# Kernel optimization log

Measured on AMD Instinct MI355X. Metric: run time of the kernel, lower is better.

The kernel has to match this reference:

```python
import jax, jax.numpy as jnp
import numpy as np

N_NODES = 100000


def _add_self_loops(edge_index, n):
    loops = jnp.arange(n, dtype=edge_index.dtype)
    src = jnp.concatenate([edge_index[0], loops])
    dst = jnp.concatenate([edge_index[1], loops])
    return src, dst


def _gcn_norm(src, dst, n):
    # symmetric normalization with unit edge weights (edge_weight=None)
    w = jnp.ones(src.shape[0], dtype=jnp.float32)
    deg = jax.ops.segment_sum(w, dst, num_segments=n)  # in-degree at dst (col)
    dinv = jnp.where(deg > 0, jax.lax.rsqrt(jnp.maximum(deg, 1.0)), 0.0)
    return dinv[src] * w * dinv[dst]


def _gcn_conv(x, W, b, src, dst, norm, n):
    h = x @ W                              # [N, F_out] linear first (as in PyG GCNConv)
    msg = h[src] * norm[:, None]           # gather + per-edge scale
    agg = jax.ops.segment_sum(msg, dst, num_segments=n)  # scatter-add at dst
    return agg + b


def setup_inputs() -> dict:
    key = jax.random.key(0)
    k1, k2, k3, k4 = jax.random.split(key, 4)
    x = jax.random.normal(k1, (N_NODES, 128), dtype=jnp.float32)
    edge_index = jax.random.randint(k2, (2, 1600000), 0, N_NODES, dtype=jnp.int64)
    W1 = jax.random.normal(k3, (128, 64), dtype=jnp.float32) * 0.08
    b1 = jnp.zeros((64,), dtype=jnp.float32)
    W2 = jax.random.normal(k4, (64, 40), dtype=jnp.float32) * 0.1
    b2 = jnp.zeros((40,), dtype=jnp.float32)
    return {"x": x, "edge_index": edge_index, "W1": W1, "b1": b1, "W2": W2, "b2": b2}


def reference(x, edge_index, W1, b1, W2, b2):
    n = x.shape[0]
    src, dst = _add_self_loops(edge_index, n)
    norm = _gcn_norm(src, dst, n)
    h = _gcn_conv(x, W1, b1, src, dst, norm, n)
    h = jax.nn.relu(h)
    # dropout is identity in eval mode (training=False)
    out = _gcn_conv(h, W2, b2, src, dst, norm, n)
    return out
```

## Files before the change

kernel.cpp:

```cpp
#include <hip/hip_runtime.h>
#include <hip/hip_fp16.h>


#define NPB   128
#define NBCAP 1024


__global__ void k_zero(int* __restrict__ p, int m) {
    int i = blockIdx.x * blockDim.x + threadIdx.x;
    if (i < m) p[i] = 0;
}

__global__ __launch_bounds__(256) void k_hist(const int* __restrict__ dst, int E,
                                              int* __restrict__ bcnt, int nb) {
    __shared__ int h[NBCAP];
    for (int i = threadIdx.x; i < nb; i += 256) h[i] = 0;
    __syncthreads();
    int stride = gridDim.x * 256;
    for (int e = blockIdx.x * 256 + threadIdx.x; e < E; e += stride)
        atomicAdd(&h[dst[e] >> 7], 1);
    __syncthreads();
    for (int i = threadIdx.x; i < nb; i += 256)
        if (h[i]) atomicAdd(&bcnt[i], h[i]);
}

__global__ __launch_bounds__(1024) void k_scan_nb(const int* __restrict__ bcnt,
                                                  int* __restrict__ bbase,
                                                  int* __restrict__ bcur, int nb) {
    __shared__ int tmp[NBCAP];
    int t = threadIdx.x;
    int v = (t < nb) ? bcnt[t] : 0;
    tmp[t] = v;
    __syncthreads();
    for (int ofs = 1; ofs < NBCAP; ofs <<= 1) {
        int u = (t >= ofs) ? tmp[t - ofs] : 0;
        __syncthreads();
        if (t >= ofs) tmp[t] += u;
        __syncthreads();
    }
    if (t < nb) {
        int ex = tmp[t] - v;
        bbase[t] = ex;
        bcur[t] = ex;
        if (t == nb - 1) bbase[nb] = tmp[t];
    }
}

__global__ __launch_bounds__(256) void k_binpass(const int* __restrict__ src,
                                                 const int* __restrict__ dst,
                                                 int* __restrict__ bcur,
                                                 int* __restrict__ pairs,
                                                 int nb, int E) {
    __shared__ int lh[NBCAP];
    __shared__ int lbase[NBCAP];
    for (int i = threadIdx.x; i < nb; i += 256) lh[i] = 0;
    __syncthreads();
    int base = blockIdx.x * 4096;
    int pk[16], bb[16];
#pragma unroll
    for (int k = 0; k < 16; ++k) {
        int e = base + k * 256 + threadIdx.x;
        if (e < E) {
            int d = dst[e];
            int b = d >> 7;
            bb[k] = b;
            pk[k] = src[e] | ((d & (NPB - 1)) << 17);
            atomicAdd(&lh[b], 1);
        } else bb[k] = -1;
    }
    __syncthreads();
    for (int i = threadIdx.x; i < nb; i += 256) {
        int c = lh[i];
        lbase[i] = c ? atomicAdd(&bcur[i], c) : 0;
        lh[i] = 0;
    }
    __syncthreads();
#pragma unroll
    for (int k = 0; k < 16; ++k) {
        if (bb[k] >= 0) {
            int r = atomicAdd(&lh[bb[k]], 1);
            pairs[lbase[bb[k]] + r] = pk[k];
        }
    }
}

__global__ __launch_bounds__(256) void k_bucket_build(const int* __restrict__ pairs,
                                                      const int* __restrict__ bbase,
                                                      int* __restrict__ off,
                                                      int* __restrict__ csrc,
                                                      float* __restrict__ dinv,
                                                      int n, int nb) {
    __shared__ int deg[NPB], sc[NPB], cur[NPB];
    int t = threadIdx.x;
    int bid = blockIdx.x;
    int node0 = bid * NPB;
    int ebeg = bbase[bid], eend = bbase[bid + 1];
    if (t < NPB) deg[t] = 0;
    __syncthreads();
    for (int e = ebeg + t; e < eend; e += 256)
        atomicAdd(&deg[pairs[e] >> 17], 1);
    __syncthreads();
    if (t < NPB) sc[t] = deg[t];
    __syncthreads();
    for (int ofs = 1; ofs < NPB; ofs <<= 1) {
        int u = (t < NPB && t >= ofs) ? sc[t - ofs] : 0;
        __syncthreads();
        if (t < NPB && t >= ofs) sc[t] += u;
        __syncthreads();
    }
    if (t < NPB) {
        int ex = sc[t] - deg[t];
        cur[t] = ex;
        int node = node0 + t;
        if (node < n) {
            off[node] = ebeg + ex;
            dinv[node] = rsqrtf((float)(deg[t] + 1));
        }
    }
    if (t == 0 && bid == nb - 1) off[n] = eend;
    __syncthreads();
    for (int e = ebeg + t; e < eend; e += 256) {
        int pkv = pairs[e];
        int r = atomicAdd(&cur[pkv >> 17], 1);
        csrc[ebeg + r] = pkv & 0x1FFFF;
    }
}


union pk2 { __half2 h[2]; uint2 u; };
union pk4 { __half2 h[4]; uint4 u; };

#define F4ADD(a, b) { (a).x += (b).x; (a).y += (b).y; (a).z += (b).z; (a).w += (b).w; }

__device__ __forceinline__ void acc8f(float4& lo, float4& hi, uint4 u) {
    __half2 h0 = *(__half2*)&u.x, h1 = *(__half2*)&u.y;
    __half2 h2v = *(__half2*)&u.z, h3v = *(__half2*)&u.w;
    float2 f0 = __half22float2(h0), f1 = __half22float2(h1);
    float2 f2 = __half22float2(h2v), f3 = __half22float2(h3v);
    lo.x += f0.x; lo.y += f0.y; lo.z += f1.x; lo.w += f1.y;
    hi.x += f2.x; hi.y += f2.y; hi.z += f3.x; hi.w += f3.y;
}

__device__ __forceinline__ void redstep(float4& lo, float4& hi, int delta, bool act) {
    float4 rl, rh;
    rl.x = __shfl_down(lo.x, delta); rl.y = __shfl_down(lo.y, delta);
    rl.z = __shfl_down(lo.z, delta); rl.w = __shfl_down(lo.w, delta);
    rh.x = __shfl_down(hi.x, delta); rh.y = __shfl_down(hi.y, delta);
    rh.z = __shfl_down(hi.z, delta); rh.w = __shfl_down(hi.w, delta);
    if (act) { F4ADD(lo, rl); F4ADD(hi, rh); }
}


__global__ __launch_bounds__(256) void k_gemm1_h(const float* __restrict__ x,
                                                 const float* __restrict__ W,
                                                 __half* __restrict__ h, int n,
                                                 const float* __restrict__ dinv) {
    __shared__ float Ws[64 * 64];
    __shared__ float xsT[64 * 64];
    const int tid = threadIdx.x;
    const int row0 = blockIdx.x * 64;
    const int tc = tid & 15;
    const int rg = tid >> 4;
    const int r = tid & 63, g = tid >> 6;
    const int row = row0 + r;

    float acc[4][4];
#pragma unroll
    for (int i = 0; i < 4; ++i)
#pragma unroll
        for (int j = 0; j < 4; ++j) acc[i][j] = 0.f;

#pragma unroll
    for (int kh = 0; kh < 2; ++kh) {
        {
            const float4* Wg = (const float4*)(W + kh * 64 * 64);
            float4* Wl = (float4*)Ws;
#pragma unroll
            for (int t = 0; t < 4; ++t) Wl[tid + t * 256] = Wg[tid + t * 256];
        }
        {
            const float4* xr = (const float4*)(x + (size_t)row * 128 + kh * 64);
#pragma unroll
            for (int t = 0; t < 4; ++t) {
                int k0 = g * 16 + t * 4;
                float4 v = (row < n) ? xr[k0 >> 2] : make_float4(0.f, 0.f, 0.f, 0.f);
                xsT[(k0 + 0) * 64 + r] = v.x;
                xsT[(k0 + 1) * 64 + r] = v.y;
                xsT[(k0 + 2) * 64 + r] = v.z;
                xsT[(k0 + 3) * 64 + r] = v.w;
            }
        }
        __syncthreads();

#pragma unroll 4
        for (int k = 0; k < 64; ++k) {
            float4 a = *(const float4*)&xsT[k * 64 + rg * 4];
            float4 b = *(const float4*)&Ws[k * 64 + tc * 4];
            acc[0][0] += a.x * b.x; acc[0][1] += a.x * b.y; acc[0][2] += a.x * b.z; acc[0][3] += a.x * b.w;
            acc[1][0] += a.y * b.x; acc[1][1] += a.y * b.y; acc[1][2] += a.y * b.z; acc[1][3] += a.y * b.w;
            acc[2][0] += a.z * b.x; acc[2][1] += a.z * b.y; acc[2][2] += a.z * b.z; acc[2][3] += a.z * b.w;
            acc[3][0] += a.w * b.x; acc[3][1] += a.w * b.y; acc[3][2] += a.w * b.z; acc[3][3] += a.w * b.w;
        }
        __syncthreads();
    }

#pragma unroll
    for (int i = 0; i < 4; ++i) {
        int orow = row0 + rg * 4 + i;
        if (orow < n) {
            float dd = dinv[orow];
            pk2 p;
            p.h[0] = __floats2half2_rn(acc[i][0] * dd, acc[i][1] * dd);
            p.h[1] = __floats2half2_rn(acc[i][2] * dd, acc[i][3] * dd);
            *(uint2*)&h[(size_t)orow * 64 + tc * 4] = p.u;
        }
    }
}

__global__ __launch_bounds__(256) void k_gemm2_out(const __half* __restrict__ g2,
                                                   const float* __restrict__ W2,
                                                   const float* __restrict__ b2,
                                                   float* __restrict__ out, int n) {
    __shared__ float Ws[64 * 40];
    __shared__ float hsT[64 * 64];
    const int tid = threadIdx.x;
    const int row0 = blockIdx.x * 64;
    {
        const float4* Wg = (const float4*)W2;
        float4* Wl = (float4*)Ws;
        for (int i = tid; i < 640; i += 256) Wl[i] = Wg[i];
    }
    {
        int r = tid & 63, g = tid >> 6;
        int row = row0 + r;
        const __half* ar = g2 + (size_t)row * 64;
#pragma unroll
        for (int t = 0; t < 4; ++t) {
            int k0 = g * 16 + t * 4;
            float4 v = make_float4(0.f, 0.f, 0.f, 0.f);
            if (row < n) {
                uint2 u = *(const uint2*)(ar + k0);
                __half2 h0 = *(__half2*)&u.x, h1 = *(__half2*)&u.y;
                float2 f0 = __half22float2(h0), f1 = __half22float2(h1);
                v = make_float4(f0.x, f0.y, f1.x, f1.y);
            }
            hsT[(k0 + 0) * 64 + r] = v.x;
            hsT[(k0 + 1) * 64 + r] = v.y;
            hsT[(k0 + 2) * 64 + r] = v.z;
            hsT[(k0 + 3) * 64 + r] = v.w;
        }
    }
    __syncthreads();

    const int tc = tid & 15;
    const int rg = tid >> 4;
    if (tc < 10) {
        float acc[4][4];
#pragma unroll
        for (int i = 0; i < 4; ++i)
#pragma unroll
            for (int j = 0; j < 4; ++j) acc[i][j] = 0.f;

#pragma unroll 4
        for (int k = 0; k < 64; ++k) {
            float4 a = *(const float4*)&hsT[k * 64 + rg * 4];
            float4 b = *(const float4*)&Ws[k * 40 + tc * 4];
            acc[0][0] += a.x * b.x; acc[0][1] += a.x * b.y; acc[0][2] += a.x * b.z; acc[0][3] += a.x * b.w;
            acc[1][0] += a.y * b.x; acc[1][1] += a.y * b.y; acc[1][2] += a.y * b.z; acc[1][3] += a.y * b.w;
            acc[2][0] += a.z * b.x; acc[2][1] += a.z * b.y; acc[2][2] += a.z * b.z; acc[2][3] += a.z * b.w;
            acc[3][0] += a.w * b.x; acc[3][1] += a.w * b.y; acc[3][2] += a.w * b.z; acc[3][3] += a.w * b.w;
        }

        float4 bb = *(const float4*)(b2 + tc * 4);
#pragma unroll
        for (int i = 0; i < 4; ++i) {
            int row = row0 + rg * 4 + i;
            if (row < n)
                *(float4*)&out[(size_t)row * 40 + tc * 4] =
                    make_float4(acc[i][0] + bb.x, acc[i][1] + bb.y,
                                acc[i][2] + bb.z, acc[i][3] + bb.w);
        }
    }
}


__global__ __launch_bounds__(256) void k_gather_h(const __half* __restrict__ feat,
                                                  const int* __restrict__ off,
                                                  const int* __restrict__ csrc,
                                                  const float* __restrict__ dinv,
                                                  const float* __restrict__ bias,
                                                  __half* __restrict__ outh,
                                                  int n, int nwaves, int mode) {
    int wid = (blockIdx.x * 256 + threadIdx.x) >> 6;
    int lane = threadIdx.x & 63;
    int g = lane >> 3, q = lane & 7;
    for (int node = wid; node < n; node += nwaves) {
        int beg = off[node], end = off[node + 1];
        float4 a0 = make_float4(0.f, 0.f, 0.f, 0.f);
        float4 a1 = make_float4(0.f, 0.f, 0.f, 0.f);
        float4 c0 = make_float4(0.f, 0.f, 0.f, 0.f);
        float4 c1 = make_float4(0.f, 0.f, 0.f, 0.f);
        int j = beg;
        for (; j + 16 <= end; j += 16) {
            int s0 = csrc[j + g];
            int s1 = csrc[j + 8 + g];
            uint4 u0 = *(const uint4*)(feat + ((size_t)s0 << 6) + (q << 3));
            uint4 u1 = *(const uint4*)(feat + ((size_t)s1 << 6) + (q << 3));
            acc8f(a0, a1, u0);
            acc8f(c0, c1, u1);
        }
        for (; j + 8 <= end; j += 8) {
            int s0 = csrc[j + g];
            uint4 u0 = *(const uint4*)(feat + ((size_t)s0 << 6) + (q << 3));
            acc8f(a0, a1, u0);
        }
        if (j + g < end) {
            int s0 = csrc[j + g];
            uint4 u0 = *(const uint4*)(feat + ((size_t)s0 << 6) + (q << 3));
            acc8f(a0, a1, u0);
        }
        F4ADD(a0, c0); F4ADD(a1, c1);
        redstep(a0, a1, 32, lane < 32);
        redstep(a0, a1, 16, lane < 16);
        redstep(a0, a1, 8,  lane < 8);
        if (lane < 8) {
            float dd = dinv[node];
            uint4 us = *(const uint4*)(feat + ((size_t)node << 6) + (q << 3));
            float4 slo = make_float4(0.f, 0.f, 0.f, 0.f);
            float4 shi = make_float4(0.f, 0.f, 0.f, 0.f);
            acc8f(slo, shi, us);
            float f0 = (a0.x + slo.x) * dd;
            float f1 = (a0.y + slo.y) * dd;
            float f2 = (a0.z + slo.z) * dd;
            float f3 = (a0.w + slo.w) * dd;
            float f4 = (a1.x + shi.x) * dd;
            float f5 = (a1.y + shi.y) * dd;
            float f6 = (a1.z + shi.z) * dd;
            float f7 = (a1.w + shi.w) * dd;
            if (mode == 0) {
                float4 blo = *(const float4*)(bias + q * 8);
                float4 bhi = *(const float4*)(bias + q * 8 + 4);
                f0 += blo.x; f1 += blo.y; f2 += blo.z; f3 += blo.w;
                f4 += bhi.x; f5 += bhi.y; f6 += bhi.z; f7 += bhi.w;
                f0 = (f0 > 0.f ? f0 : 0.f) * dd;
                f1 = (f1 > 0.f ? f1 : 0.f) * dd;
                f2 = (f2 > 0.f ? f2 : 0.f) * dd;
                f3 = (f3 > 0.f ? f3 : 0.f) * dd;
                f4 = (f4 > 0.f ? f4 : 0.f) * dd;
                f5 = (f5 > 0.f ? f5 : 0.f) * dd;
                f6 = (f6 > 0.f ? f6 : 0.f) * dd;
                f7 = (f7 > 0.f ? f7 : 0.f) * dd;
            }
            pk4 p;
            p.h[0] = __floats2half2_rn(f0, f1);
            p.h[1] = __floats2half2_rn(f2, f3);
            p.h[2] = __floats2half2_rn(f4, f5);
            p.h[3] = __floats2half2_rn(f6, f7);
            *(uint4*)&outh[((size_t)node << 6) + (q << 3)] = p.u;
        }
    }
}


__global__ void k_init_deg(float* __restrict__ deg, int n) {
    int i = blockIdx.x * blockDim.x + threadIdx.x;
    if (i < n) deg[i] = 1.0f;
}

__global__ void k_deg(const int* __restrict__ dst, int E, float* __restrict__ deg) {
    int i = blockIdx.x * blockDim.x + threadIdx.x;
    if (i < E) atomicAdd(&deg[dst[i]], 1.0f);
}

__global__ void k_rsqrt(float* __restrict__ deg, int n) {
    int i = blockIdx.x * blockDim.x + threadIdx.x;
    if (i < n) deg[i] = rsqrtf(deg[i]);
}

__global__ __launch_bounds__(256) void k_gemm1_f(const float* __restrict__ x,
                                                 const float* __restrict__ W,
                                                 float* __restrict__ h, int n) {
    __shared__ float Ws[128 * 64];
    __shared__ float xsT[128 * 64];
    const int tid = threadIdx.x;
    const int row0 = blockIdx.x * 64;
    {
        const float4* Wg = (const float4*)W;
        float4* Wl = (float4*)Ws;
#pragma unroll
        for (int t = 0; t < 8; ++t) Wl[tid + t * 256] = Wg[tid + t * 256];
    }
    {
        int r = tid & 63, g = tid >> 6;
        int row = row0 + r;
        const float4* xr = (const float4*)(x + (size_t)row * 128);
#pragma unroll
        for (int t = 0; t < 8; ++t) {
            int k0 = g * 32 + t * 4;
            float4 v = (row < n) ? xr[k0 >> 2] : make_float4(0.f, 0.f, 0.f, 0.f);
            xsT[(k0 + 0) * 64 + r] = v.x;
            xsT[(k0 + 1) * 64 + r] = v.y;
            xsT[(k0 + 2) * 64 + r] = v.z;
            xsT[(k0 + 3) * 64 + r] = v.w;
        }
    }
    __syncthreads();
    const int tc = tid & 15;
    const int rg = tid >> 4;
    float acc[4][4];
#pragma unroll
    for (int i = 0; i < 4; ++i)
#pragma unroll
        for (int j = 0; j < 4; ++j) acc[i][j] = 0.f;
#pragma unroll 4
    for (int k = 0; k < 128; ++k) {
        float4 a = *(const float4*)&xsT[k * 64 + rg * 4];
        float4 b = *(const float4*)&Ws[k * 64 + tc * 4];
        acc[0][0] += a.x * b.x; acc[0][1] += a.x * b.y; acc[0][2] += a.x * b.z; acc[0][3] += a.x * b.w;
        acc[1][0] += a.y * b.x; acc[1][1] += a.y * b.y; acc[1][2] += a.y * b.z; acc[1][3] += a.y * b.w;
        acc[2][0] += a.z * b.x; acc[2][1] += a.z * b.y; acc[2][2] += a.z * b.z; acc[2][3] += a.z * b.w;
        acc[3][0] += a.w * b.x; acc[3][1] += a.w * b.y; acc[3][2] += a.w * b.z; acc[3][3] += a.w * b.w;
    }
#pragma unroll
    for (int i = 0; i < 4; ++i) {
        int row = row0 + rg * 4 + i;
        if (row < n)
            *(float4*)&h[(size_t)row * 64 + tc * 4] =
                make_float4(acc[i][0], acc[i][1], acc[i][2], acc[i][3]);
    }
}

__global__ __launch_bounds__(256) void k_gemm2_f(const float* __restrict__ agg,
                                                 const float* __restrict__ W2,
                                                 float* __restrict__ h2, int n) {
    __shared__ float Ws[64 * 40];
    __shared__ float hsT[64 * 64];
    const int tid = threadIdx.x;
    const int row0 = blockIdx.x * 64;
    {
        const float4* Wg = (const float4*)W2;
        float4* Wl = (float4*)Ws;
        for (int i = tid; i < 640; i += 256) Wl[i] = Wg[i];
    }
    {
        int r = tid & 63, g = tid >> 6;
        int row = row0 + r;
        const float4* ar = (const float4*)(agg + (size_t)row * 64);
#pragma unroll
        for (int t = 0; t < 4; ++t) {
            int k0 = g * 16 + t * 4;
            float4 v = (row < n) ? ar[k0 >> 2] : make_float4(0.f, 0.f, 0.f, 0.f);
            hsT[(k0 + 0) * 64 + r] = v.x > 0.f ? v.x : 0.f;
            hsT[(k0 + 1) * 64 + r] = v.y > 0.f ? v.y : 0.f;
            hsT[(k0 + 2) * 64 + r] = v.z > 0.f ? v.z : 0.f;
            hsT[(k0 + 3) * 64 + r] = v.w > 0.f ? v.w : 0.f;
        }
    }
    __syncthreads();
    const int tc = tid & 15;
    const int rg = tid >> 4;
    if (tc < 10) {
        float acc[4][4];
#pragma unroll
        for (int i = 0; i < 4; ++i)
#pragma unroll
            for (int j = 0; j < 4; ++j) acc[i][j] = 0.f;
#pragma unroll 4
        for (int k = 0; k < 64; ++k) {
            float4 a = *(const float4*)&hsT[k * 64 + rg * 4];
            float4 b = *(const float4*)&Ws[k * 40 + tc * 4];
            acc[0][0] += a.x * b.x; acc[0][1] += a.x * b.y; acc[0][2] += a.x * b.z; acc[0][3] += a.x * b.w;
            acc[1][0] += a.y * b.x; acc[1][1] += a.y * b.y; acc[1][2] += a.y * b.z; acc[1][3] += a.y * b.w;
            acc[2][0] += a.z * b.x; acc[2][1] += a.z * b.y; acc[2][2] += a.z * b.z; acc[2][3] += a.z * b.w;
            acc[3][0] += a.w * b.x; acc[3][1] += a.w * b.y; acc[3][2] += a.w * b.z; acc[3][3] += a.w * b.w;
        }
#pragma unroll
        for (int i = 0; i < 4; ++i) {
            int row = row0 + rg * 4 + i;
            if (row < n)
                *(float4*)&h2[(size_t)row * 40 + tc * 4] =
                    make_float4(acc[i][0], acc[i][1], acc[i][2], acc[i][3]);
        }
    }
}

__global__ void k_init_agg1(const float* __restrict__ h, const float* __restrict__ dinv,
                            const float* __restrict__ b1, float* __restrict__ agg, int n) {
    int idx = blockIdx.x * blockDim.x + threadIdx.x;
    if (idx < n * 64) {
        int i = idx >> 6, f = idx & 63;
        float d = dinv[i];
        agg[idx] = h[idx] * d * d + b1[f];
    }
}

__global__ __launch_bounds__(256) void k_scatter1(const float* __restrict__ h,
                                                  const int* __restrict__ src,
                                                  const int* __restrict__ dst,
                                                  const float* __restrict__ dinv,
                                                  float* __restrict__ agg, int E) {
    int e = blockIdx.x * 4 + (threadIdx.x >> 6);
    if (e >= E) return;
    int f = threadIdx.x & 63;
    int s = src[e], d = dst[e];
    float w = dinv[s] * dinv[d];
    atomicAdd(&agg[d * 64 + f], h[s * 64 + f] * w);
}

__global__ void k_init_out(const float* __restrict__ h2, const float* __restrict__ dinv,
                           const float* __restrict__ b2, float* __restrict__ out, int n) {
    int idx = blockIdx.x * blockDim.x + threadIdx.x;
    if (idx < n * 40) {
        int i = idx / 40;
        int f = idx - i * 40;
        float d = dinv[i];
        out[idx] = h2[idx] * d * d + b2[f];
    }
}

__global__ __launch_bounds__(256) void k_scatter2(const float* __restrict__ h2,
                                                  const int* __restrict__ src,
                                                  const int* __restrict__ dst,
                                                  const float* __restrict__ dinv,
                                                  float* __restrict__ out, int E) {
    int idx = blockIdx.x * blockDim.x + threadIdx.x;
    int total = E * 40;
    if (idx >= total) return;
    int e = idx / 40;
    int f = idx - e * 40;
    int s = src[e], d = dst[e];
    float w = dinv[s] * dinv[d];
    atomicAdd(&out[d * 40 + f], h2[s * 40 + f] * w);
}

extern "C" void kernel_launch(void* const* d_in, const int* in_sizes, int n_in,
                              void* d_out, int out_size, void* d_ws, size_t ws_size,
                              hipStream_t stream) {
    const float* x  = (const float*)d_in[0];
    const int*   ei = (const int*)d_in[1];
    const float* W1 = (const float*)d_in[2];
    const float* b1 = (const float*)d_in[3];
    const float* W2 = (const float*)d_in[4];
    const float* b2 = (const float*)d_in[5];
    float* out = (float*)d_out;

    const int n = in_sizes[0] / 128;
    const int E = in_sizes[1] / 2;
    const int* src = ei;
    const int* dst = ei + E;

    char* ws = (char*)d_ws;
    const size_t MB = 1 << 20;
    float*  dinv   = (float*)(ws);
    int*    off    = (int*)  (ws + 512 * 1024);
    int*    bcnt   = (int*)  (ws + 1 * MB);
    int*    bbase  = (int*)  (ws + 1 * MB + 8 * 1024);
    int*    bcur   = (int*)  (ws + 1 * MB + 16 * 1024);
    __half* hs_h   = (__half*)(ws + 2 * MB);
    __half* r2_h   = (__half*)(ws + 15 * MB);
    __half* g2_h   = hs_h;
    int*    pairs  = (int*)  (ws + 28 * MB);
    int*    csrc   = (int*)  (ws + 35 * MB);
    size_t needed_fast = 35 * MB + (size_t)E * 4;

    const int nb = (n + NPB - 1) / NPB;

    if (ws_size >= needed_fast && nb <= NBCAP && n <= (1 << 17)) {
        k_zero<<<(nb + 255) / 256, 256, 0, stream>>>(bcnt, nb);
        k_hist<<<512, 256, 0, stream>>>(dst, E, bcnt, nb);
        k_scan_nb<<<1, 1024, 0, stream>>>(bcnt, bbase, bcur, nb);
        k_binpass<<<(E + 4095) / 4096, 256, 0, stream>>>(src, dst, bcur, pairs, nb, E);
        k_bucket_build<<<nb, 256, 0, stream>>>(pairs, bbase, off, csrc, dinv, n, nb);

        const int GB = 2048;
        const int NW = GB * 4;

        k_gemm1_h<<<(n + 63) / 64, 256, 0, stream>>>(x, W1, hs_h, n, dinv);
        k_gather_h<<<GB, 256, 0, stream>>>(hs_h, off, csrc, dinv, b1, r2_h, n, NW, 0);

        k_gather_h<<<GB, 256, 0, stream>>>(r2_h, off, csrc, dinv, b1, g2_h, n, NW, 1);
        k_gemm2_out<<<(n + 63) / 64, 256, 0, stream>>>(g2_h, W2, b2, out, n);
    } else {
        float* hlin = (float*)(ws + 2 * MB);
        float* agg1 = (float*)(ws + 28 * MB);
        k_init_deg<<<(n + 255) / 256, 256, 0, stream>>>(dinv, n);
        k_deg<<<(E + 255) / 256, 256, 0, stream>>>(dst, E, dinv);
        k_rsqrt<<<(n + 255) / 256, 256, 0, stream>>>(dinv, n);
        k_gemm1_f<<<(n + 63) / 64, 256, 0, stream>>>(x, W1, hlin, n);
        k_init_agg1<<<(n * 64 + 255) / 256, 256, 0, stream>>>(hlin, dinv, b1, agg1, n);
        k_scatter1<<<(E + 3) / 4, 256, 0, stream>>>(hlin, src, dst, dinv, agg1, E);
        k_gemm2_f<<<(n + 63) / 64, 256, 0, stream>>>(agg1, W2, hlin, n);
        k_init_out<<<(n * 40 + 255) / 256, 256, 0, stream>>>(hlin, dinv, b2, out, n);
        int total2 = E * 40;
        k_scatter2<<<(total2 + 255) / 256, 256, 0, stream>>>(hlin, src, dst, dinv, out, E);
    }
}
```

Before: 187.1 us.

## Double bucket size to 256 nodes and pre-sum gathered fp16 pairs

Measured after the change: 186.4 us. About the same (-0.3%).

```diff
diff --git a/kernel.cpp b/kernel.cpp
--- a/kernel.cpp
+++ b/kernel.cpp
@@ -2,8 +2,9 @@
 #include <hip/hip_fp16.h>
 
 
-#define NPB   128
-#define NBCAP 1024
+#define NPB      256
+#define NB_SHIFT 8
+#define NBCAP    512
 
 
 __global__ void k_zero(int* __restrict__ p, int m) {
@@ -18,21 +19,21 @@
     __syncthreads();
     int stride = gridDim.x * 256;
     for (int e = blockIdx.x * 256 + threadIdx.x; e < E; e += stride)
-        atomicAdd(&h[dst[e] >> 7], 1);
+        atomicAdd(&h[dst[e] >> NB_SHIFT], 1);
     __syncthreads();
     for (int i = threadIdx.x; i < nb; i += 256)
         if (h[i]) atomicAdd(&bcnt[i], h[i]);
 }
 
-__global__ __launch_bounds__(1024) void k_scan_nb(const int* __restrict__ bcnt,
-                                                  int* __restrict__ bbase,
-                                                  int* __restrict__ bcur, int nb) {
-    __shared__ int tmp[NBCAP];
+__global__ __launch_bounds__(512) void k_scan_nb(const int* __restrict__ bcnt,
+                                                 int* __restrict__ bbase,
+                                                 int* __restrict__ bcur, int nb) {
+    __shared__ int tmp[512];
     int t = threadIdx.x;
     int v = (t < nb) ? bcnt[t] : 0;
     tmp[t] = v;
     __syncthreads();
-    for (int ofs = 1; ofs < NBCAP; ofs <<= 1) {
+    for (int ofs = 1; ofs < 512; ofs <<= 1) {
         int u = (t >= ofs) ? tmp[t - ofs] : 0;
         __syncthreads();
         if (t >= ofs) tmp[t] += u;
@@ -62,7 +63,7 @@
         int e = base + k * 256 + threadIdx.x;
         if (e < E) {
             int d = dst[e];
-            int b = d >> 7;
+            int b = d >> NB_SHIFT;
             bb[k] = b;
             pk[k] = src[e] | ((d & (NPB - 1)) << 17);
             atomicAdd(&lh[b], 1);
@@ -95,20 +96,20 @@
     int bid = blockIdx.x;
     int node0 = bid * NPB;
     int ebeg = bbase[bid], eend = bbase[bid + 1];
-    if (t < NPB) deg[t] = 0;
+    deg[t] = 0;
     __syncthreads();
     for (int e = ebeg + t; e < eend; e += 256)
         atomicAdd(&deg[pairs[e] >> 17], 1);
     __syncthreads();
-    if (t < NPB) sc[t] = deg[t];
+    sc[t] = deg[t];
     __syncthreads();
     for (int ofs = 1; ofs < NPB; ofs <<= 1) {
-        int u = (t < NPB && t >= ofs) ? sc[t - ofs] : 0;
+        int u = (t >= ofs) ? sc[t - ofs] : 0;
         __syncthreads();
-        if (t < NPB && t >= ofs) sc[t] += u;
+        if (t >= ofs) sc[t] += u;
         __syncthreads();
     }
-    if (t < NPB) {
+    {
         int ex = sc[t] - deg[t];
         cur[t] = ex;
         int node = node0 + t;
@@ -139,6 +140,16 @@
     float2 f2 = __half22float2(h2v), f3 = __half22float2(h3v);
     lo.x += f0.x; lo.y += f0.y; lo.z += f1.x; lo.w += f1.y;
     hi.x += f2.x; hi.y += f2.y; hi.z += f3.x; hi.w += f3.y;
+}
+
+__device__ __forceinline__ uint4 hpadd(uint4 a, uint4 b) {
+    pk4 pa, pb, pr;
+    pa.u = a; pb.u = b;
+    pr.h[0] = __hadd2(pa.h[0], pb.h[0]);
+    pr.h[1] = __hadd2(pa.h[1], pb.h[1]);
+    pr.h[2] = __hadd2(pa.h[2], pb.h[2]);
+    pr.h[3] = __hadd2(pa.h[3], pb.h[3]);
+    return pr.u;
 }
 
 __device__ __forceinline__ void redstep(float4& lo, float4& hi, int delta, bool act) {
@@ -298,16 +309,13 @@
         int beg = off[node], end = off[node + 1];
         float4 a0 = make_float4(0.f, 0.f, 0.f, 0.f);
         float4 a1 = make_float4(0.f, 0.f, 0.f, 0.f);
-        float4 c0 = make_float4(0.f, 0.f, 0.f, 0.f);
-        float4 c1 = make_float4(0.f, 0.f, 0.f, 0.f);
         int j = beg;
         for (; j + 16 <= end; j += 16) {
             int s0 = csrc[j + g];
             int s1 = csrc[j + 8 + g];
             uint4 u0 = *(const uint4*)(feat + ((size_t)s0 << 6) + (q << 3));
             uint4 u1 = *(const uint4*)(feat + ((size_t)s1 << 6) + (q << 3));
-            acc8f(a0, a1, u0);
-            acc8f(c0, c1, u1);
+            acc8f(a0, a1, hpadd(u0, u1));
         }
         for (; j + 8 <= end; j += 8) {
             int s0 = csrc[j + g];
@@ -319,7 +327,6 @@
             uint4 u0 = *(const uint4*)(feat + ((size_t)s0 << 6) + (q << 3));
             acc8f(a0, a1, u0);
         }
-        F4ADD(a0, c0); F4ADD(a1, c1);
         redstep(a0, a1, 32, lane < 32);
         redstep(a0, a1, 16, lane < 16);
         redstep(a0, a1, 8,  lane < 8);
@@ -568,7 +575,7 @@
     if (ws_size >= needed_fast && nb <= NBCAP && n <= (1 << 17)) {
         k_zero<<<(nb + 255) / 256, 256, 0, stream>>>(bcnt, nb);
         k_hist<<<512, 256, 0, stream>>>(dst, E, bcnt, nb);
-        k_scan_nb<<<1, 1024, 0, stream>>>(bcnt, bbase, bcur, nb);
+        k_scan_nb<<<1, 512, 0, stream>>>(bcnt, bbase, bcur, nb);
         k_binpass<<<(E + 4095) / 4096, 256, 0, stream>>>(src, dst, bcur, pairs, nb, E);
         k_bucket_build<<<nb, 256, 0, stream>>>(pairs, bbase, off, csrc, dinv, n, nb);
 
```
